# Kernel optimization log

Measured on AMD Instinct MI355X. Metric: run time of the kernel, lower is better.

## Reference

```python
import jax, jax.numpy as jnp
import numpy as np

S = 7          # side
B = 2          # boxes per cell
C = 20         # classes
L = S * S      # grid cells
NOOBJ = 0.5 * 1.0
OBJ   = 0.5 * 1.0
CLS   = 0.5 * 1.0
COORD = 0.5 * 5.0


def setup_inputs() -> dict:
    key = jax.random.key(0)
    k1, k2, k3 = jax.random.split(key, 3)
    n = 16384
    preds = jax.random.uniform(k1, (n, L * (C + 5 * B)), dtype=jnp.float32)
    labels = jax.random.uniform(k2, (n, L * (1 + C + 4)), dtype=jnp.float32)
    lab = labels.reshape(n, L, 1 + C + 4)
    obj_flag = (jax.random.uniform(k3, (n, L)) < 0.15).astype(jnp.float32)
    lab = lab.at[:, :, 0].set(obj_flag)
    labels = lab.reshape(n, -1)
    return {"preds": preds, "labels": labels}


def _iou(t, o):
    # t, o: [..., 4] boxes in (cx, cy, w, h); returns [...]
    left   = jnp.maximum(t[..., 0] - 0.5 * t[..., 2], o[..., 0] - 0.5 * o[..., 2])
    right  = jnp.minimum(t[..., 0] + 0.5 * t[..., 2], o[..., 0] + 0.5 * o[..., 2])
    top    = jnp.maximum(t[..., 1] - 0.5 * t[..., 3], o[..., 1] - 0.5 * o[..., 3])
    bottom = jnp.minimum(t[..., 1] + 0.5 * t[..., 3], o[..., 1] + 0.5 * o[..., 3])
    w = right - left
    h = bottom - top
    invalid = (w < 0) | (h < 0)
    inter = jnp.where(invalid, 0.0, w * h)
    union = t[..., 2] * t[..., 3] + o[..., 2] * o[..., 3] - inter
    return jnp.where(invalid, 0.0, inter / jnp.maximum(union, 1e-12))


def reference(preds, labels):
    n = preds.shape[0]
    pcls  = preds[:, : L * C].reshape(n, L, C)                       # [n,L,C]
    pconf = preds[:, L * C : L * C + L * B].reshape(n, L, B)          # [n,L,B]
    pbox  = preds[:, L * C + L * B :].reshape(n, L, B, 4)             # [n,L,B,4]

    lab  = labels.reshape(n, L, 1 + C + 4)
    obj  = lab[:, :, 0] != 0                                          # [n,L]
    tcls = lab[:, :, 1 : 1 + C]                                       # [n,L,C]
    tbox = lab[:, :, 1 + C :]                                         # [n,L,4] raw

    # --- best-box selection (on detached predictions, like .detach() in torch) ---
    o_raw = jax.lax.stop_gradient(pbox)
    o = jnp.concatenate([o_raw[..., :2] / S, o_raw[..., 2:] ** 2], axis=-1)      # [n,L,B,4]
    t = jnp.concatenate([tbox[..., :2] / S, tbox[..., 2:]], axis=-1)[:, :, None] # [n,L,1,4]
    t = jax.lax.stop_gradient(t)

    iou  = _iou(t, o)                                                 # [n,L,B]
    rmse = jnp.sqrt(jnp.sum((t - o) ** 2, axis=-1))                   # [n,L,B]
    max_iou = jnp.max(iou, axis=-1)
    # if any IoU>0 pick first argmax of IoU, else first argmin of RMSE (best_rmse init 20)
    best = jnp.where(max_iou > 0, jnp.argmax(iou, axis=-1), jnp.argmin(rmse, axis=-1))  # [n,L]
    best_iou = jnp.take_along_axis(iou, best[:, :, None], axis=-1)[..., 0]        # [n,L]

    onehot = jnp.arange(B) == best[:, :, None]                        # [n,L,B]
    mask_best = obj[:, :, None] & onehot

    # confidence delta: noobject everywhere, overwritten at best box of object cells
    conf_delta = jnp.where(mask_best,
                           OBJ * (best_iou[:, :, None] - pconf) ** 2,
                           NOOBJ * pconf ** 2)

    # class delta (object cells only)
    cls_delta = jnp.where(obj[:, :, None], CLS * (tcls - pcls) ** 2, 0.0)

    # coord delta at best box: raw truth x,y and sqrt(truth w,h) vs raw preds
    pbest = jnp.take_along_axis(pbox, best[:, :, None, None], axis=2)[:, :, 0]    # [n,L,4]
    ttarget = jnp.concatenate([tbox[..., :2], jnp.sqrt(tbox[..., 2:])], axis=-1)  # [n,L,4]
    coord_delta = jnp.where(obj[:, :, None], COORD * (ttarget - pbest) ** 2, 0.0)

    return jnp.nansum(conf_delta) + jnp.nansum(cls_delta) + jnp.nansum(coord_delta)
```

## Files before the change

kernel.cpp:

```cpp
#include <hip/hip_runtime.h>


#define L_CELLS 49
#define PRED_ROW 1470
#define LAB_ROW 1225
#define CONF_BASE 980
#define BOX_BASE 1078
#define W_NOOBJ 0.5f
#define W_OBJ 0.5f
#define W_CLS 0.5f
#define W_COORD 2.5f
#define INV_S (1.0f / 7.0f)

#define LAB_SLOTS 308
#define WAVE_SLOTS 310

__global__ __launch_bounds__(256, 6) void yolo_loss_kernel(
    const float* __restrict__ preds, const float* __restrict__ labels,
    float* __restrict__ ws) {
  __shared__ float4 st[4][WAVE_SLOTS];

  const int tid = threadIdx.x;
  const int w = tid >> 6;
  const int lane = tid & 63;
  const int s = blockIdx.x * 4 + w;
  float4* stw = st[w];

  size_t g0 = (size_t)s * LAB_ROW;
  size_t ga = g0 & ~(size_t)3;
  int loff = (int)(g0 - ga);
#pragma unroll
  for (int r = 0; r < 5; ++r) {
    int i = lane + 64 * r;
    if (i < LAB_SLOTS) stw[i] = *(const float4*)(labels + ga + 4 * (size_t)i);
  }

  const float* lab = (const float*)stw + loff;
  const float* rp = preds + (size_t)s * PRED_ROW;

  float acc = 0.0f;
  if (lane < L_CELLS) {
    const int l = lane;
    float2 cf = *(const float2*)(rp + CONF_BASE + 2 * l);
    float c0v = cf.x, c1v = cf.y;
    float objf = lab[25 * l];

    if (objf != 0.0f) {
      float bx[8];
#pragma unroll
      for (int k = 0; k < 4; ++k) {
        float2 b2 = *(const float2*)(rp + BOX_BASE + 8 * l + 2 * k);
        bx[2 * k] = b2.x;
        bx[2 * k + 1] = b2.y;
      }
      float tx = lab[25 * l + 21], ty = lab[25 * l + 22];
      float tw = lab[25 * l + 23], th = lab[25 * l + 24];
      float t0 = tx * INV_S, t1 = ty * INV_S, t2 = tw, t3 = th;

      float iou[2], rmse2[2];
#pragma unroll
      for (int b = 0; b < 2; ++b) {
        float o0 = bx[4 * b + 0] * INV_S;
        float o1 = bx[4 * b + 1] * INV_S;
        float o2 = bx[4 * b + 2] * bx[4 * b + 2];
        float o3 = bx[4 * b + 3] * bx[4 * b + 3];
        float left = fmaxf(t0 - 0.5f * t2, o0 - 0.5f * o2);
        float right = fminf(t0 + 0.5f * t2, o0 + 0.5f * o2);
        float top = fmaxf(t1 - 0.5f * t3, o1 - 0.5f * o3);
        float bot = fminf(t1 + 0.5f * t3, o1 + 0.5f * o3);
        float wd = right - left;
        float h = bot - top;
        bool invalid = (wd < 0.0f) || (h < 0.0f);
        float inter = invalid ? 0.0f : wd * h;
        float uni = t2 * t3 + o2 * o3 - inter;
        iou[b] = invalid ? 0.0f : inter / fmaxf(uni, 1e-12f);
        float d0 = t0 - o0, d1 = t1 - o1, d2 = t2 - o2, d3 = t3 - o3;
        rmse2[b] = d0 * d0 + d1 * d1 + d2 * d2 + d3 * d3;
      }

      float max_iou = fmaxf(iou[0], iou[1]);
      int best;
      if (max_iou > 0.0f)
        best = (iou[1] > iou[0]) ? 1 : 0;
      else
        best = (rmse2[1] < rmse2[0]) ? 1 : 0;
      float best_iou = iou[best];

      float cb = (best == 0) ? c0v : c1v;
      float co = (best == 0) ? c1v : c0v;
      float db = best_iou - cb;
      acc += W_OBJ * db * db + W_NOOBJ * co * co;

      float clsacc = 0.0f;
#pragma unroll
      for (int k = 0; k < 10; ++k) {
        float2 p = *(const float2*)(rp + 20 * l + 2 * k);
        float d0 = lab[25 * l + 1 + 2 * k] - p.x;
        float d1 = lab[25 * l + 2 + 2 * k] - p.y;
        clsacc += d0 * d0 + d1 * d1;
      }
      acc += W_CLS * clsacc;

      float e0 = tx - bx[best * 4 + 0];
      float e1 = ty - bx[best * 4 + 1];
      float e2 = sqrtf(tw) - bx[best * 4 + 2];
      float e3 = sqrtf(th) - bx[best * 4 + 3];
      acc += W_COORD * (e0 * e0 + e1 * e1 + e2 * e2 + e3 * e3);
    } else {
      acc += W_NOOBJ * (c0v * c0v + c1v * c1v);
    }
  }

#pragma unroll
  for (int o = 32; o > 0; o >>= 1) acc += __shfl_down(acc, o);

  __shared__ float wsum[4];
  if (lane == 0) wsum[w] = acc;
  __syncthreads();
  if (tid == 0) ws[blockIdx.x] = wsum[0] + wsum[1] + wsum[2] + wsum[3];
}

__global__ __launch_bounds__(1024) void final_reduce_kernel(
    const float* __restrict__ ws, float* __restrict__ out, int m) {
  float acc = 0.0f;
  for (int i = threadIdx.x; i < m; i += 1024) acc += ws[i];
#pragma unroll
  for (int o = 32; o > 0; o >>= 1) acc += __shfl_down(acc, o);
  __shared__ float wsum[16];
  int wave = threadIdx.x >> 6;
  int lane = threadIdx.x & 63;
  if (lane == 0) wsum[wave] = acc;
  __syncthreads();
  if (threadIdx.x == 0) {
    float sum = 0.0f;
#pragma unroll
    for (int i = 0; i < 16; ++i) sum += wsum[i];
    out[0] = sum;
  }
}

extern "C" void kernel_launch(void* const* d_in, const int* in_sizes, int n_in,
                              void* d_out, int out_size, void* d_ws, size_t ws_size,
                              hipStream_t stream) {
  const float* preds = (const float*)d_in[0];
  const float* labels = (const float*)d_in[1];
  float* out = (float*)d_out;
  float* ws = (float*)d_ws;
  int n = in_sizes[0] / PRED_ROW;
  int blocks = n / 4;

  yolo_loss_kernel<<<blocks, 256, 0, stream>>>(preds, labels, ws);
  final_reduce_kernel<<<1, 1024, 0, stream>>>(ws, out, blocks);
}
```

Baseline: 185.3 us.

## Stage labels via global_load_lds and issue all prediction loads up front branchlessly

Label rows are copied straight into LDS with the async global_load_lds builtin instead of passing through registers. All prediction loads (confidence, class, box) are issued before one wait, and the object/no-object branch becomes a select, so the whole wave shares one memory latency. The cost is loading class and box data for every cell, including the roughly 85% without objects, which raises memory traffic. Launch bounds drop from 6 to 5 blocks per CU to make room for the extra registers.

```diff
diff --git a/kernel.cpp b/kernel.cpp
--- a/kernel.cpp
+++ b/kernel.cpp
@@ -15,7 +15,10 @@
 #define LAB_SLOTS 308
 #define WAVE_SLOTS 310
 
-__global__ __launch_bounds__(256, 6) void yolo_loss_kernel(
+typedef int __attribute__((address_space(1))) as1_int;
+typedef int __attribute__((address_space(3))) as3_int;
+
+__global__ __launch_bounds__(256, 5) void yolo_loss_kernel(
     const float* __restrict__ preds, const float* __restrict__ labels,
     float* __restrict__ ws) {
   __shared__ float4 st[4][WAVE_SLOTS];
@@ -32,83 +35,98 @@
 #pragma unroll
   for (int r = 0; r < 5; ++r) {
     int i = lane + 64 * r;
-    if (i < LAB_SLOTS) stw[i] = *(const float4*)(labels + ga + 4 * (size_t)i);
+    if (i < LAB_SLOTS) {
+      __builtin_amdgcn_global_load_lds(
+          (const as1_int*)(labels + ga + 4 * (size_t)i),
+          (as3_int*)((float*)stw + 256 * r), 16, 0, 0);
+    }
   }
 
+  const float* rp = preds + (size_t)s * PRED_ROW;
+
+  float2 cf = make_float2(0.f, 0.f);
+  float2 pc[10];
+  float2 bq[4];
+  if (lane < L_CELLS) {
+    const int l = lane;
+    cf = *(const float2*)(rp + CONF_BASE + 2 * l);
+#pragma unroll
+    for (int k = 0; k < 10; ++k)
+      pc[k] = *(const float2*)(rp + 20 * l + 2 * k);
+#pragma unroll
+    for (int k = 0; k < 4; ++k)
+      bq[k] = *(const float2*)(rp + BOX_BASE + 8 * l + 2 * k);
+  }
+
+  asm volatile("s_waitcnt vmcnt(0)" ::: "memory");
+  __builtin_amdgcn_sched_barrier(0);
+
   const float* lab = (const float*)stw + loff;
-  const float* rp = preds + (size_t)s * PRED_ROW;
 
   float acc = 0.0f;
   if (lane < L_CELLS) {
     const int l = lane;
-    float2 cf = *(const float2*)(rp + CONF_BASE + 2 * l);
     float c0v = cf.x, c1v = cf.y;
     float objf = lab[25 * l];
 
-    if (objf != 0.0f) {
-      float bx[8];
+    float noobj_term = W_NOOBJ * (c0v * c0v + c1v * c1v);
+
+    float bx[8] = {bq[0].x, bq[0].y, bq[1].x, bq[1].y,
+                   bq[2].x, bq[2].y, bq[3].x, bq[3].y};
+    float tx = lab[25 * l + 21], ty = lab[25 * l + 22];
+    float tw = lab[25 * l + 23], th = lab[25 * l + 24];
+    float t0 = tx * INV_S, t1 = ty * INV_S, t2 = tw, t3 = th;
+
+    float iou[2], rmse2[2];
 #pragma unroll
-      for (int k = 0; k < 4; ++k) {
-        float2 b2 = *(const float2*)(rp + BOX_BASE + 8 * l + 2 * k);
-        bx[2 * k] = b2.x;
-        bx[2 * k + 1] = b2.y;
-      }
-      float tx = lab[25 * l + 21], ty = lab[25 * l + 22];
-      float tw = lab[25 * l + 23], th = lab[25 * l + 24];
-      float t0 = tx * INV_S, t1 = ty * INV_S, t2 = tw, t3 = th;
+    for (int b = 0; b < 2; ++b) {
+      float o0 = bx[4 * b + 0] * INV_S;
+      float o1 = bx[4 * b + 1] * INV_S;
+      float o2 = bx[4 * b + 2] * bx[4 * b + 2];
+      float o3 = bx[4 * b + 3] * bx[4 * b + 3];
+      float left = fmaxf(t0 - 0.5f * t2, o0 - 0.5f * o2);
+      float right = fminf(t0 + 0.5f * t2, o0 + 0.5f * o2);
+      float top = fmaxf(t1 - 0.5f * t3, o1 - 0.5f * o3);
+      float bot = fminf(t1 + 0.5f * t3, o1 + 0.5f * o3);
+      float wd = right - left;
+      float h = bot - top;
+      bool invalid = (wd < 0.0f) || (h < 0.0f);
+      float inter = invalid ? 0.0f : wd * h;
+      float uni = t2 * t3 + o2 * o3 - inter;
+      iou[b] = invalid ? 0.0f : inter / fmaxf(uni, 1e-12f);
+      float d0 = t0 - o0, d1 = t1 - o1, d2 = t2 - o2, d3 = t3 - o3;
+      rmse2[b] = d0 * d0 + d1 * d1 + d2 * d2 + d3 * d3;
+    }
 
-      float iou[2], rmse2[2];
+    float max_iou = fmaxf(iou[0], iou[1]);
+    int best;
+    if (max_iou > 0.0f)
+      best = (iou[1] > iou[0]) ? 1 : 0;
+    else
+      best = (rmse2[1] < rmse2[0]) ? 1 : 0;
+    float best_iou = iou[best];
+
+    float cb = (best == 0) ? c0v : c1v;
+    float co = (best == 0) ? c1v : c0v;
+    float db = best_iou - cb;
+    float obj_term = W_OBJ * db * db + W_NOOBJ * co * co;
+
+    float clsacc = 0.0f;
 #pragma unroll
-      for (int b = 0; b < 2; ++b) {
-        float o0 = bx[4 * b + 0] * INV_S;
-        float o1 = bx[4 * b + 1] * INV_S;
-        float o2 = bx[4 * b + 2] * bx[4 * b + 2];
-        float o3 = bx[4 * b + 3] * bx[4 * b + 3];
-        float left = fmaxf(t0 - 0.5f * t2, o0 - 0.5f * o2);
-        float right = fminf(t0 + 0.5f * t2, o0 + 0.5f * o2);
-        float top = fmaxf(t1 - 0.5f * t3, o1 - 0.5f * o3);
-        float bot = fminf(t1 + 0.5f * t3, o1 + 0.5f * o3);
-        float wd = right - left;
-        float h = bot - top;
-        bool invalid = (wd < 0.0f) || (h < 0.0f);
-        float inter = invalid ? 0.0f : wd * h;
-        float uni = t2 * t3 + o2 * o3 - inter;
-        iou[b] = invalid ? 0.0f : inter / fmaxf(uni, 1e-12f);
-        float d0 = t0 - o0, d1 = t1 - o1, d2 = t2 - o2, d3 = t3 - o3;
-        rmse2[b] = d0 * d0 + d1 * d1 + d2 * d2 + d3 * d3;
-      }
+    for (int k = 0; k < 10; ++k) {
+      float d0 = lab[25 * l + 1 + 2 * k] - pc[k].x;
+      float d1 = lab[25 * l + 2 + 2 * k] - pc[k].y;
+      clsacc += d0 * d0 + d1 * d1;
+    }
+    obj_term += W_CLS * clsacc;
 
-      float max_iou = fmaxf(iou[0], iou[1]);
-      int best;
-      if (max_iou > 0.0f)
-        best = (iou[1] > iou[0]) ? 1 : 0;
-      else
-        best = (rmse2[1] < rmse2[0]) ? 1 : 0;
-      float best_iou = iou[best];
+    float e0 = tx - bx[best * 4 + 0];
+    float e1 = ty - bx[best * 4 + 1];
+    float e2 = sqrtf(tw) - bx[best * 4 + 2];
+    float e3 = sqrtf(th) - bx[best * 4 + 3];
+    obj_term += W_COORD * (e0 * e0 + e1 * e1 + e2 * e2 + e3 * e3);
 
-      float cb = (best == 0) ? c0v : c1v;
-      float co = (best == 0) ? c1v : c0v;
-      float db = best_iou - cb;
-      acc += W_OBJ * db * db + W_NOOBJ * co * co;
-
-      float clsacc = 0.0f;
-#pragma unroll
-      for (int k = 0; k < 10; ++k) {
-        float2 p = *(const float2*)(rp + 20 * l + 2 * k);
-        float d0 = lab[25 * l + 1 + 2 * k] - p.x;
-        float d1 = lab[25 * l + 2 + 2 * k] - p.y;
-        clsacc += d0 * d0 + d1 * d1;
-      }
-      acc += W_CLS * clsacc;
-
-      float e0 = tx - bx[best * 4 + 0];
-      float e1 = ty - bx[best * 4 + 1];
-      float e2 = sqrtf(tw) - bx[best * 4 + 2];
-      float e3 = sqrtf(th) - bx[best * 4 + 3];
-      acc += W_COORD * (e0 * e0 + e1 * e1 + e2 * e2 + e3 * e3);
-    } else {
-      acc += W_NOOBJ * (c0v * c0v + c1v * c1v);
-    }
+    acc = (objf != 0.0f) ? obj_term : noobj_term;
   }
 
 #pragma unroll
```

Result: slower. 190.2 us (+2.6%).
